# Kernel tuning notes

Measured on AMD Instinct MI355X. Metric: run time of the kernel, lower is better.

The kernel has to match this reference:

```python
import jax, jax.numpy as jnp
import numpy as np

N = 50000      # nodes
E = 400000     # directed edges
F_IN = 128     # input features
H0, C0 = 4, 64     # layer0: 4 heads x 64, concat -> 256
H1, C1 = 1, 256    # layer1: 1 head x 256, mean/concat -> 256
NCLS = 10
SLOPE = 0.2    # PyG GATConv leaky_relu negative_slope


def setup_inputs() -> dict:
    key = jax.random.key(0)
    ks = jax.random.split(key, 20)
    g = lambda k, shape, fan_in: jax.random.normal(k, shape, jnp.float32) * (1.0 / np.sqrt(fan_in))
    x = jax.random.normal(ks[0], (N, F_IN), jnp.float32)
    edge_index = jax.random.randint(ks[1], (2, E), 0, N)
    return {
        "x": x,
        "edge_index": edge_index,
        # GATConv layer 0: 128 -> 4 heads x 64, concat
        "W0": g(ks[2], (F_IN, H0 * C0), F_IN),
        "a_src0": g(ks[3], (H0, C0), C0),
        "a_dst0": g(ks[4], (H0, C0), C0),
        "b0": jnp.zeros((H0 * C0,), jnp.float32),
        # GATConv layer 1: 256 -> 1 head x 256, averaged
        "W1": g(ks[5], (H0 * C0, H1 * C1), H0 * C0),
        "a_src1": g(ks[6], (H1, C1), C1),
        "a_dst1": g(ks[7], (H1, C1), C1),
        "b1": jnp.zeros((C1,), jnp.float32),
        # MLP head 256 -> 512 -> 1024 -> NCLS
        "lw1": g(ks[8], (256, 512), 256), "lb1": jnp.zeros((512,), jnp.float32),
        "lw2": g(ks[9], (512, 1024), 512), "lb2": jnp.zeros((1024,), jnp.float32),
        "lw3": g(ks[10], (1024, NCLS), 1024), "lb3": jnp.zeros((NCLS,), jnp.float32),
    }


def _gat_conv(x, src, dst, valid, W, a_src, a_dst, b, heads, ch, concat):
    """PyG GATConv (eval mode, dropout=0): gather -> edge attention ->
    softmax over incoming edges per target -> scatter-sum aggregate."""
    n = x.shape[0]
    h = (x @ W).reshape(n, heads, ch)                      # [N,H,C]
    alpha_src = jnp.sum(h * a_src[None], axis=-1)          # [N,H]
    alpha_dst = jnp.sum(h * a_dst[None], axis=-1)          # [N,H]
    e = jax.nn.leaky_relu(alpha_src[src] + alpha_dst[dst], SLOPE)  # [Etot,H]
    e = jnp.where(valid[:, None], e, -1e9)                 # removed self-loops
    emax = jax.lax.stop_gradient(jax.ops.segment_max(e, dst, num_segments=n))
    w = jnp.exp(e - emax[dst]) * valid[:, None].astype(e.dtype)
    denom = jax.ops.segment_sum(w, dst, num_segments=n)    # [N,H] (>0: self-loops)
    w = w / denom[dst]
    out = jax.ops.segment_sum(h[src] * w[..., None], dst, num_segments=n)  # [N,H,C]
    out = out.reshape(n, heads * ch) if concat else out.mean(axis=1)
    return out + b


def reference(x, edge_index, W0, a_src0, a_dst0, b0, W1, a_src1, a_dst1, b1,
              lw1, lb1, lw2, lb2, lw3, lb3):
    n = x.shape[0]
    s0, d0 = edge_index[0], edge_index[1]
    loop = jnp.arange(n, dtype=s0.dtype)
    src = jnp.concatenate([s0, loop])
    dst = jnp.concatenate([d0, loop])
    valid = jnp.concatenate([s0 != d0, jnp.ones((n,), bool)])  # remove+add self-loops
    h = jax.nn.relu(_gat_conv(x, src, dst, valid, W0, a_src0, a_dst0, b0, H0, C0, True))
    h = jax.nn.relu(_gat_conv(h, src, dst, valid, W1, a_src1, a_dst1, b1, H1, C1, False))
    h = jax.nn.relu(h @ lw1 + lb1)
    h = jax.nn.relu(h @ lw2 + lb2)
    h = jax.nn.relu(h @ lw3 + lb3)
    return jax.nn.softmax(h, axis=1)
```

## Files before the change

### kernel.cpp

```cpp
#include <hip/hip_runtime.h>
#include <cstdint>
#include <cstddef>

#define F_IN   128
#define SLOPE  0.2f

typedef unsigned short u16;
typedef __attribute__((ext_vector_type(8))) short     bf16x8;
typedef __attribute__((ext_vector_type(8))) unsigned short u16x8;
typedef __attribute__((ext_vector_type(4))) unsigned short u16x4;
typedef __attribute__((ext_vector_type(4))) float     f32x4;

__device__ __forceinline__ u16 f2bf(float f) {
    unsigned u = __float_as_uint(f);
    unsigned r = u + 0x7FFFu + ((u >> 16) & 1u);
    return (u16)(r >> 16);
}
__device__ __forceinline__ float bf2f(u16 h) {
    return __uint_as_float(((unsigned)h) << 16);
}

__device__ __forceinline__ float lrelu(float v) { return v >= 0.f ? v : SLOPE * v; }

__global__ void alphas0_k(const u16* __restrict__ h0, const float* __restrict__ a_src,
                          const float* __restrict__ a_dst, float* __restrict__ asrc,
                          float* __restrict__ adst, int N) {
    int gid = blockIdx.x * blockDim.x + threadIdx.x;
    int n = gid >> 6, lane = gid & 63;
    if (n >= N) return;
    #pragma unroll
    for (int h = 0; h < 4; ++h) {
        float v  = bf2f(h0[(size_t)n * 256 + h * 64 + lane]);
        float s1 = v * a_src[h * 64 + lane];
        float s2 = v * a_dst[h * 64 + lane];
        #pragma unroll
        for (int off = 32; off; off >>= 1) {
            s1 += __shfl_down(s1, off);
            s2 += __shfl_down(s2, off);
        }
        if (lane == 0) { asrc[n * 4 + h] = s1; adst[n * 4 + h] = s2; }
    }
}

__global__ void alphas1_k(const u16* __restrict__ h1, const float* __restrict__ a_src,
                          const float* __restrict__ a_dst, float* __restrict__ asrc,
                          float* __restrict__ adst, int N) {
    int gid = blockIdx.x * blockDim.x + threadIdx.x;
    int n = gid >> 6, lane = gid & 63;
    if (n >= N) return;
    float s1 = 0.f, s2 = 0.f;
    #pragma unroll
    for (int k = 0; k < 4; ++k) {
        float v = bf2f(h1[(size_t)n * 256 + k * 64 + lane]);
        s1 += v * a_src[k * 64 + lane];
        s2 += v * a_dst[k * 64 + lane];
    }
    #pragma unroll
    for (int off = 32; off; off >>= 1) {
        s1 += __shfl_down(s1, off);
        s2 += __shfl_down(s2, off);
    }
    if (lane == 0) { asrc[n] = s1; adst[n] = s2; }
}

__global__ void deg_init(int* __restrict__ deg, int N) {
    int i = blockIdx.x * blockDim.x + threadIdx.x;
    if (i < N) deg[i] = 1;
}

__global__ void count_deg(const int* __restrict__ ei, int* __restrict__ deg, int E) {
    int e = blockIdx.x * blockDim.x + threadIdx.x;
    if (e >= E) return;
    int s = ei[e], d = ei[E + e];
    if (s != d) atomicAdd(&deg[d], 1);
}

__global__ void scan1(const int* __restrict__ deg, int* __restrict__ part,
                      int* __restrict__ bsum, int N) {
    __shared__ int sm[256];
    int i = blockIdx.x * 256 + threadIdx.x;
    int v = (i < N) ? deg[i] : 0;
    sm[threadIdx.x] = v; __syncthreads();
    for (int off = 1; off < 256; off <<= 1) {
        int tv = (threadIdx.x >= off) ? sm[threadIdx.x - off] : 0;
        __syncthreads();
        sm[threadIdx.x] += tv;
        __syncthreads();
    }
    if (i < N) part[i] = sm[threadIdx.x] - v;
    if (threadIdx.x == 255) bsum[blockIdx.x] = sm[255];
}

__global__ void scan2(int* __restrict__ bsum, int nb) {
    __shared__ int sm[256];
    __shared__ int carry;
    if (threadIdx.x == 0) carry = 0;
    __syncthreads();
    for (int base = 0; base < nb; base += 256) {
        int i = base + threadIdx.x;
        int v = (i < nb) ? bsum[i] : 0;
        sm[threadIdx.x] = v; __syncthreads();
        for (int off = 1; off < 256; off <<= 1) {
            int tv = (threadIdx.x >= off) ? sm[threadIdx.x - off] : 0;
            __syncthreads();
            sm[threadIdx.x] += tv;
            __syncthreads();
        }
        if (i < nb) bsum[i] = sm[threadIdx.x] - v + carry;
        __syncthreads();
        if (threadIdx.x == 0) carry += sm[255];
        __syncthreads();
    }
}

__global__ void scan3(const int* __restrict__ deg, const int* __restrict__ part,
                      const int* __restrict__ bsum, int* __restrict__ rowp,
                      int* __restrict__ cursor, int N) {
    int i = blockIdx.x * blockDim.x + threadIdx.x;
    if (i >= N) return;
    int r = part[i] + bsum[i >> 8];
    rowp[i] = r;
    cursor[i] = r;
    if (i == N - 1) rowp[N] = r + deg[i];
}

__global__ void scatter_k(const int* __restrict__ ei, int* __restrict__ cursor,
                          int* __restrict__ csr, int E, int N) {
    int e = blockIdx.x * blockDim.x + threadIdx.x;
    if (e >= E + N) return;
    int s, d;
    if (e < E) { s = ei[e]; d = ei[E + e]; if (s == d) return; }
    else       { s = d = e - E; }
    int pos = atomicAdd(&cursor[d], 1);
    csr[pos] = s;
}

__global__ void gat_gather0(const int* __restrict__ csr, const int* __restrict__ rowp,
                            const u16* __restrict__ h0, const float* __restrict__ asrc,
                            const float* __restrict__ adst, const float* __restrict__ b,
                            float* __restrict__ outx, int N) {
    int gid = blockIdx.x * blockDim.x + threadIdx.x;
    int n = gid >> 6, lane = gid & 63;
    if (n >= N) return;
    int beg = rowp[n], end = rowp[n + 1];
    float4 ad = *(const float4*)(adst + (size_t)n * 4);
    float m0 = -1e30f, m1 = -1e30f, m2 = -1e30f, m3 = -1e30f;
    for (int i = beg + lane; i < end; i += 64) {
        int s = csr[i];
        float4 as = *(const float4*)(asrc + (size_t)s * 4);
        m0 = fmaxf(m0, lrelu(as.x + ad.x));
        m1 = fmaxf(m1, lrelu(as.y + ad.y));
        m2 = fmaxf(m2, lrelu(as.z + ad.z));
        m3 = fmaxf(m3, lrelu(as.w + ad.w));
    }
    #pragma unroll
    for (int off = 32; off; off >>= 1) {
        m0 = fmaxf(m0, __shfl_xor(m0, off));
        m1 = fmaxf(m1, __shfl_xor(m1, off));
        m2 = fmaxf(m2, __shfl_xor(m2, off));
        m3 = fmaxf(m3, __shfl_xor(m3, off));
    }
    float acc0 = 0.f, acc1 = 0.f, acc2 = 0.f, acc3 = 0.f;
    float den0 = 0.f, den1 = 0.f, den2 = 0.f, den3 = 0.f;
    for (int i = beg; i < end; ++i) {
        int s = csr[i];
        float4 as = *(const float4*)(asrc + (size_t)s * 4);
        float w0 = __expf(lrelu(as.x + ad.x) - m0);
        float w1 = __expf(lrelu(as.y + ad.y) - m1);
        float w2 = __expf(lrelu(as.z + ad.z) - m2);
        float w3 = __expf(lrelu(as.w + ad.w) - m3);
        den0 += w0; den1 += w1; den2 += w2; den3 += w3;
        const u16* hs = h0 + (size_t)s * 256;
        acc0 += w0 * bf2f(hs[lane]);
        acc1 += w1 * bf2f(hs[64 + lane]);
        acc2 += w2 * bf2f(hs[128 + lane]);
        acc3 += w3 * bf2f(hs[192 + lane]);
    }
    float* po = outx + (size_t)n * 256;
    float v;
    v = acc0 / den0 + b[lane];       po[lane]       = v > 0.f ? v : 0.f;
    v = acc1 / den1 + b[64 + lane];  po[64 + lane]  = v > 0.f ? v : 0.f;
    v = acc2 / den2 + b[128 + lane]; po[128 + lane] = v > 0.f ? v : 0.f;
    v = acc3 / den3 + b[192 + lane]; po[192 + lane] = v > 0.f ? v : 0.f;
}

__global__ void gat_gather1(const int* __restrict__ csr, const int* __restrict__ rowp,
                            const u16* __restrict__ h1, const float* __restrict__ asrc,
                            const float* __restrict__ adst, const float* __restrict__ b,
                            u16* __restrict__ outx, int N) {
    int gid = blockIdx.x * blockDim.x + threadIdx.x;
    int n = gid >> 6, lane = gid & 63;
    if (n >= N) return;
    int beg = rowp[n], end = rowp[n + 1];
    float adn = adst[n];
    float mx = -1e30f;
    for (int i = beg + lane; i < end; i += 64) {
        int s = csr[i];
        mx = fmaxf(mx, lrelu(asrc[s] + adn));
    }
    #pragma unroll
    for (int off = 32; off; off >>= 1) mx = fmaxf(mx, __shfl_xor(mx, off));
    float acc0 = 0.f, acc1 = 0.f, acc2 = 0.f, acc3 = 0.f, den = 0.f;
    for (int i = beg; i < end; ++i) {
        int s = csr[i];
        float w = __expf(lrelu(asrc[s] + adn) - mx);
        den += w;
        const u16* hs = h1 + (size_t)s * 256;
        acc0 += w * bf2f(hs[lane]);
        acc1 += w * bf2f(hs[64 + lane]);
        acc2 += w * bf2f(hs[128 + lane]);
        acc3 += w * bf2f(hs[192 + lane]);
    }
    float inv = 1.f / den;
    u16* po = outx + (size_t)n * 256;
    float v;
    v = acc0 * inv + b[lane];       po[lane]       = f2bf(v > 0.f ? v : 0.f);
    v = acc1 * inv + b[64 + lane];  po[64 + lane]  = f2bf(v > 0.f ? v : 0.f);
    v = acc2 * inv + b[128 + lane]; po[128 + lane] = f2bf(v > 0.f ? v : 0.f);
    v = acc3 * inv + b[192 + lane]; po[192 + lane] = f2bf(v > 0.f ? v : 0.f);
}

__global__ void pack_w(const float* __restrict__ W, u16* __restrict__ out,
                       int K, int Nsrc, int NT) {
    int gid  = blockIdx.x * blockDim.x + threadIdx.x;
    int lane = gid & 63, frag = gid >> 6;
    int KT = K >> 5;
    if (frag >= KT * NT) return;
    int nt = frag % NT, kt = frag / NT;
    int n  = nt * 16 + (lane & 15);
    int k0 = kt * 32 + ((lane >> 4) << 3);
    u16x8 v8;
    #pragma unroll
    for (int i = 0; i < 8; ++i) {
        float v = (n < Nsrc) ? W[(size_t)(k0 + i) * Nsrc + n] : 0.f;
        v8[i] = f2bf(v);
    }
    *(u16x8*)(out + (size_t)(frag * 64 + lane) * 8) = v8;
}

__global__ void pack_w_hl(const float* __restrict__ W, u16* __restrict__ ohi,
                          u16* __restrict__ olo, int K, int Nsrc, int NT) {
    int gid  = blockIdx.x * blockDim.x + threadIdx.x;
    int lane = gid & 63, frag = gid >> 6;
    int KT = K >> 5;
    if (frag >= KT * NT) return;
    int nt = frag % NT, kt = frag / NT;
    int n  = nt * 16 + (lane & 15);
    int k0 = kt * 32 + ((lane >> 4) << 3);
    u16x8 h8, l8;
    #pragma unroll
    for (int i = 0; i < 8; ++i) {
        float v = (n < Nsrc) ? W[(size_t)(k0 + i) * Nsrc + n] : 0.f;
        u16 hi = f2bf(v);
        h8[i] = hi;
        l8[i] = f2bf(v - bf2f(hi));
    }
    *(u16x8*)(ohi + (size_t)(frag * 64 + lane) * 8) = h8;
    *(u16x8*)(olo + (size_t)(frag * 64 + lane) * 8) = l8;
}

__device__ __forceinline__ bf16x8 lds_afrag(const u16* buf, int Kdim, int row0, int kt, int lane) {
    int row = row0 + (lane & 15);
    int k   = kt * 32 + ((lane >> 4) << 3);
    int idx = (row * Kdim + k) ^ ((row & 7) << 3);
    return *(const bf16x8*)(buf + idx);
}

__global__ __launch_bounds__(512) void gemm_mfma(
    const float* __restrict__ A, const u16* __restrict__ bhi, const u16* __restrict__ blo,
    u16* __restrict__ C, int M, int K) {
    __shared__ __align__(16) u16 Ahi[64 * 256];
    __shared__ __align__(16) u16 Alo[64 * 256];
    int t = threadIdx.x, lane = t & 63, w = t >> 6;
    int row0 = blockIdx.x * 64;
    int K4 = K >> 2;

    for (int idx = t; idx < 64 * K4; idx += 512) {
        int row = idx / K4, kq = (idx % K4) << 2;
        int gr = row0 + row;
        float4 v = make_float4(0.f, 0.f, 0.f, 0.f);
        if (gr < M) v = *(const float4*)(A + (size_t)gr * K + kq);
        u16x4 h4, l4;
        float vv[4] = {v.x, v.y, v.z, v.w};
        #pragma unroll
        for (int i = 0; i < 4; ++i) {
            u16 hi = f2bf(vv[i]);
            h4[i] = hi;
            l4[i] = f2bf(vv[i] - bf2f(hi));
        }
        int sidx = (row * K + kq) ^ ((row & 7) << 3);
        *(u16x4*)(Ahi + sidx) = h4;
        *(u16x4*)(Alo + sidx) = l4;
    }
    __syncthreads();

    int KT = K >> 5;
    f32x4 acc[4][2] = {};
    for (int kt = 0; kt < KT; ++kt) {
        bf16x8 ah[4], al[4];
        #pragma unroll
        for (int mt = 0; mt < 4; ++mt) {
            ah[mt] = lds_afrag(Ahi, K, mt * 16, kt, lane);
            al[mt] = lds_afrag(Alo, K, mt * 16, kt, lane);
        }
        #pragma unroll
        for (int nt = 0; nt < 2; ++nt) {
            int ntg = w * 2 + nt;
            size_t fo = ((size_t)(kt * 16 + ntg) * 64 + lane) * 8;
            bf16x8 bh = *(const bf16x8*)(bhi + fo);
            bf16x8 bl = *(const bf16x8*)(blo + fo);
            #pragma unroll
            for (int mt = 0; mt < 4; ++mt) {
                acc[mt][nt] = __builtin_amdgcn_mfma_f32_16x16x32_bf16(al[mt], bh, acc[mt][nt], 0, 0, 0);
                acc[mt][nt] = __builtin_amdgcn_mfma_f32_16x16x32_bf16(ah[mt], bl, acc[mt][nt], 0, 0, 0);
                acc[mt][nt] = __builtin_amdgcn_mfma_f32_16x16x32_bf16(ah[mt], bh, acc[mt][nt], 0, 0, 0);
            }
        }
    }

    #pragma unroll
    for (int mt = 0; mt < 4; ++mt)
        #pragma unroll
        for (int nt = 0; nt < 2; ++nt) {
            int col = w * 32 + nt * 16 + (lane & 15);
            #pragma unroll
            for (int j = 0; j < 4; ++j) {
                int gr = row0 + mt * 16 + ((lane >> 4) << 2) + j;
                if (gr < M) C[(size_t)gr * 256 + col] = f2bf(acc[mt][nt][j]);
            }
        }
}

#define NB 32

__global__ __launch_bounds__(1024) void mlp_mfma(
    const u16* __restrict__ m0,
    const u16* __restrict__ w1p, const float* __restrict__ lb1,
    const u16* __restrict__ w2p, const float* __restrict__ lb2,
    const u16* __restrict__ w3p, const float* __restrict__ lb3,
    float* __restrict__ out, int N) {
    __shared__ __align__(16) u16 ldsA0[32 * 256];
    __shared__ __align__(16) u16 ldsA1[32 * 512];
    __shared__ __align__(16) u16 ldsA2[32 * 1024];
    __shared__ float slog[32 * 16];

    int t = threadIdx.x, lane = t & 63, w = t >> 6;
    int nb = blockIdx.x * NB;

    if (t < 512) slog[t] = 0.f;

    {
        int row = t >> 5, kb = (t & 31) << 3;
        int gn = nb + row;
        u16x8 v8;
        if (gn < N) v8 = *(const u16x8*)(m0 + (size_t)gn * 256 + kb);
        else        v8 = (u16x8)0;
        int idx = (row * 256 + kb) ^ ((row & 7) << 3);
        *(u16x8*)(ldsA0 + idx) = v8;
    }
    __syncthreads();

    f32x4 acc1[2][2] = {};
    for (int kt = 0; kt < 8; ++kt) {
        bf16x8 a0 = lds_afrag(ldsA0, 256, 0,  kt, lane);
        bf16x8 a1 = lds_afrag(ldsA0, 256, 16, kt, lane);
        #pragma unroll
        for (int nt = 0; nt < 2; ++nt) {
            int ntg = w * 2 + nt;
            bf16x8 b = *(const bf16x8*)(w1p + ((size_t)(kt * 32 + ntg) * 64 + lane) * 8);
            acc1[0][nt] = __builtin_amdgcn_mfma_f32_16x16x32_bf16(a0, b, acc1[0][nt], 0, 0, 0);
            acc1[1][nt] = __builtin_amdgcn_mfma_f32_16x16x32_bf16(a1, b, acc1[1][nt], 0, 0, 0);
        }
    }
    #pragma unroll
    for (int mt = 0; mt < 2; ++mt)
        #pragma unroll
        for (int nt = 0; nt < 2; ++nt) {
            int col = w * 32 + nt * 16 + (lane & 15);
            float bv = lb1[col];
            #pragma unroll
            for (int j = 0; j < 4; ++j) {
                int row = mt * 16 + ((lane >> 4) << 2) + j;
                float v = acc1[mt][nt][j] + bv;
                v = v > 0.f ? v : 0.f;
                ldsA1[(row * 512 + col) ^ ((row & 7) << 3)] = f2bf(v);
            }
        }
    __syncthreads();

    f32x4 acc2[2][4] = {};
    for (int kt = 0; kt < 16; ++kt) {
        bf16x8 a0 = lds_afrag(ldsA1, 512, 0,  kt, lane);
        bf16x8 a1 = lds_afrag(ldsA1, 512, 16, kt, lane);
        #pragma unroll
        for (int nt = 0; nt < 4; ++nt) {
            int ntg = w * 4 + nt;
            bf16x8 b = *(const bf16x8*)(w2p + ((size_t)(kt * 64 + ntg) * 64 + lane) * 8);
            acc2[0][nt] = __builtin_amdgcn_mfma_f32_16x16x32_bf16(a0, b, acc2[0][nt], 0, 0, 0);
            acc2[1][nt] = __builtin_amdgcn_mfma_f32_16x16x32_bf16(a1, b, acc2[1][nt], 0, 0, 0);
        }
    }
    #pragma unroll
    for (int mt = 0; mt < 2; ++mt)
        #pragma unroll
        for (int nt = 0; nt < 4; ++nt) {
            int col = w * 64 + nt * 16 + (lane & 15);
            float bv = lb2[col];
            #pragma unroll
            for (int j = 0; j < 4; ++j) {
                int row = mt * 16 + ((lane >> 4) << 2) + j;
                float v = acc2[mt][nt][j] + bv;
                v = v > 0.f ? v : 0.f;
                ldsA2[(row * 1024 + col) ^ ((row & 7) << 3)] = f2bf(v);
            }
        }
    __syncthreads();

    {
        f32x4 acc[2] = {};
        #pragma unroll
        for (int kk = 0; kk < 2; ++kk) {
            int kt = w * 2 + kk;
            bf16x8 b3 = *(const bf16x8*)(w3p + ((size_t)kt * 64 + lane) * 8);
            bf16x8 a0 = lds_afrag(ldsA2, 1024, 0,  kt, lane);
            bf16x8 a1 = lds_afrag(ldsA2, 1024, 16, kt, lane);
            acc[0] = __builtin_amdgcn_mfma_f32_16x16x32_bf16(a0, b3, acc[0], 0, 0, 0);
            acc[1] = __builtin_amdgcn_mfma_f32_16x16x32_bf16(a1, b3, acc[1], 0, 0, 0);
        }
        int col = lane & 15;
        #pragma unroll
        for (int mt = 0; mt < 2; ++mt)
            #pragma unroll
            for (int j = 0; j < 4; ++j) {
                int row = mt * 16 + ((lane >> 4) << 2) + j;
                atomicAdd(&slog[row * 16 + col], acc[mt][j]);
            }
    }
    __syncthreads();

    if (t < 32) {
        int gn = nb + t;
        if (gn < N) {
            float lg[10], m = -1e30f;
            #pragma unroll
            for (int k = 0; k < 10; ++k) {
                float v = slog[t * 16 + k] + lb3[k];
                v = v > 0.f ? v : 0.f;
                lg[k] = v;
                if (v > m) m = v;
            }
            float ssum = 0.f;
            #pragma unroll
            for (int k = 0; k < 10; ++k) { lg[k] = __expf(lg[k] - m); ssum += lg[k]; }
            float inv = 1.f / ssum;
            #pragma unroll
            for (int k = 0; k < 10; ++k) out[(size_t)gn * 10 + k] = lg[k] * inv;
        }
    }
}

extern "C" void kernel_launch(void* const* d_in, const int* in_sizes, int n_in,
                              void* d_out, int out_size, void* d_ws, size_t ws_size,
                              hipStream_t stream) {
    const float* x       = (const float*)d_in[0];
    const int*   ei      = (const int*)  d_in[1];
    const float* W0      = (const float*)d_in[2];
    const float* a_src0  = (const float*)d_in[3];
    const float* a_dst0  = (const float*)d_in[4];
    const float* b0      = (const float*)d_in[5];
    const float* W1      = (const float*)d_in[6];
    const float* a_src1  = (const float*)d_in[7];
    const float* a_dst1  = (const float*)d_in[8];
    const float* b1      = (const float*)d_in[9];
    const float* lw1     = (const float*)d_in[10];
    const float* lb1     = (const float*)d_in[11];
    const float* lw2     = (const float*)d_in[12];
    const float* lb2     = (const float*)d_in[13];
    const float* lw3     = (const float*)d_in[14];
    const float* lb3     = (const float*)d_in[15];
    float*       out     = (float*)d_out;

    const int N  = in_sizes[0] / F_IN;
    const int E  = in_sizes[1] / 2;
    const int ET = E + N;

    char* base = (char*)d_ws;
    size_t szHb = (size_t)N * 256 * sizeof(u16);
    u16*   hbf  = (u16*)base;
    float* bufG = (float*)(base + szHb);
    u16*   m0b  = (u16*)(base + szHb + (size_t)N * 256 * sizeof(float));
    float* asrc = (float*)(base + 2 * szHb + (size_t)N * 256 * sizeof(float));
    float* adst = asrc + (size_t)N * 4;
    u16*   w1p  = (u16*)(adst + (size_t)N * 4);
    u16*   w2p  = w1p + 256 * 512;
    u16*   w3p  = w2p + 512 * 1024;
    u16*   w0h  = w3p + 1024 * 16;
    u16*   w0l  = w0h + 128 * 256;
    u16*   w1h  = w0l + 128 * 256;
    u16*   w1l  = w1h + 256 * 256;
    int*   deg  = (int*)(w1l + 256 * 256);
    int*   rowp   = deg + N;
    int*   cursor = rowp + N + 1;
    int*   part   = cursor + N;
    int*   bsum   = part + N;
    int*   csr    = bsum + 256;

    const int TB  = 256;
    const int nb1 = (N + 255) / 256;
    const int gemm_grid = (N + 63) / 64;

    pack_w<<<(8  * 32 * 64 + TB - 1) / TB, TB, 0, stream>>>(lw1, w1p, 256,  512,  32);
    pack_w<<<(16 * 64 * 64 + TB - 1) / TB, TB, 0, stream>>>(lw2, w2p, 512,  1024, 64);
    pack_w<<<(32 * 1  * 64 + TB - 1) / TB, TB, 0, stream>>>(lw3, w3p, 1024, 10,   1);
    pack_w_hl<<<(4 * 16 * 64 + TB - 1) / TB, TB, 0, stream>>>(W0, w0h, w0l, 128, 256, 16);
    pack_w_hl<<<(8 * 16 * 64 + TB - 1) / TB, TB, 0, stream>>>(W1, w1h, w1l, 256, 256, 16);

    deg_init<<<nb1, TB, 0, stream>>>(deg, N);
    count_deg<<<(E + TB - 1) / TB, TB, 0, stream>>>(ei, deg, E);
    scan1<<<nb1, TB, 0, stream>>>(deg, part, bsum, N);
    scan2<<<1, TB, 0, stream>>>(bsum, nb1);
    scan3<<<nb1, TB, 0, stream>>>(deg, part, bsum, rowp, cursor, N);
    scatter_k<<<(ET + TB - 1) / TB, TB, 0, stream>>>(ei, cursor, csr, E, N);

    gemm_mfma<<<gemm_grid, 512, 0, stream>>>(x, w0h, w0l, hbf, N, 128);
    alphas0_k<<<(N * 64 + TB - 1) / TB, TB, 0, stream>>>(hbf, a_src0, a_dst0, asrc, adst, N);
    gat_gather0<<<((size_t)N * 64 + TB - 1) / TB, TB, 0, stream>>>(csr, rowp, hbf, asrc, adst, b0, bufG, N);

    gemm_mfma<<<gemm_grid, 512, 0, stream>>>(bufG, w1h, w1l, hbf, N, 256);
    alphas1_k<<<(N * 64 + TB - 1) / TB, TB, 0, stream>>>(hbf, a_src1, a_dst1, asrc, adst, N);
    gat_gather1<<<((size_t)N * 64 + TB - 1) / TB, TB, 0, stream>>>(csr, rowp, hbf, asrc, adst, b1, m0b, N);

    mlp_mfma<<<(N + NB - 1) / NB, 1024, 0, stream>>>(m0b, w1p, lb1, w2p, lb2, w3p, lb3, out, N);
}
```

Measured before the change: 458.3 us.

## Chunk MLP layer2 output and fuse layer3 per chunk, halving block size

```diff
diff --git a/kernel.cpp b/kernel.cpp
--- a/kernel.cpp
+++ b/kernel.cpp
@@ -333,107 +333,115 @@
 
 #define NB 32
 
-__global__ __launch_bounds__(1024) void mlp_mfma(
+__global__ __launch_bounds__(512) void mlp_mfma(
     const u16* __restrict__ m0,
     const u16* __restrict__ w1p, const float* __restrict__ lb1,
     const u16* __restrict__ w2p, const float* __restrict__ lb2,
     const u16* __restrict__ w3p, const float* __restrict__ lb3,
     float* __restrict__ out, int N) {
-    __shared__ __align__(16) u16 ldsA0[32 * 256];
+    __shared__ __align__(16) u16 ldsIn[32 * 256];
     __shared__ __align__(16) u16 ldsA1[32 * 512];
-    __shared__ __align__(16) u16 ldsA2[32 * 1024];
     __shared__ float slog[32 * 16];
 
     int t = threadIdx.x, lane = t & 63, w = t >> 6;
     int nb = blockIdx.x * NB;
 
-    if (t < 512) slog[t] = 0.f;
-
-    {
-        int row = t >> 5, kb = (t & 31) << 3;
+    slog[t] = 0.f;
+
+    #pragma unroll
+    for (int u = 0; u < 2; ++u) {
+        int unit = t + u * 512;
+        int row = unit >> 5, kb = (unit & 31) << 3;
         int gn = nb + row;
         u16x8 v8;
         if (gn < N) v8 = *(const u16x8*)(m0 + (size_t)gn * 256 + kb);
         else        v8 = (u16x8)0;
         int idx = (row * 256 + kb) ^ ((row & 7) << 3);
-        *(u16x8*)(ldsA0 + idx) = v8;
+        *(u16x8*)(ldsIn + idx) = v8;
     }
     __syncthreads();
 
-    f32x4 acc1[2][2] = {};
-    for (int kt = 0; kt < 8; ++kt) {
-        bf16x8 a0 = lds_afrag(ldsA0, 256, 0,  kt, lane);
-        bf16x8 a1 = lds_afrag(ldsA0, 256, 16, kt, lane);
-        #pragma unroll
-        for (int nt = 0; nt < 2; ++nt) {
-            int ntg = w * 2 + nt;
-            bf16x8 b = *(const bf16x8*)(w1p + ((size_t)(kt * 32 + ntg) * 64 + lane) * 8);
-            acc1[0][nt] = __builtin_amdgcn_mfma_f32_16x16x32_bf16(a0, b, acc1[0][nt], 0, 0, 0);
-            acc1[1][nt] = __builtin_amdgcn_mfma_f32_16x16x32_bf16(a1, b, acc1[1][nt], 0, 0, 0);
-        }
-    }
-    #pragma unroll
-    for (int mt = 0; mt < 2; ++mt)
-        #pragma unroll
-        for (int nt = 0; nt < 2; ++nt) {
-            int col = w * 32 + nt * 16 + (lane & 15);
-            float bv = lb1[col];
+    {
+        f32x4 acc1[2][4] = {};
+        for (int kt = 0; kt < 8; ++kt) {
+            bf16x8 a0 = lds_afrag(ldsIn, 256, 0,  kt, lane);
+            bf16x8 a1 = lds_afrag(ldsIn, 256, 16, kt, lane);
+            #pragma unroll
+            for (int nt = 0; nt < 4; ++nt) {
+                int ntg = w * 4 + nt;
+                bf16x8 b = *(const bf16x8*)(w1p + ((size_t)(kt * 32 + ntg) * 64 + lane) * 8);
+                acc1[0][nt] = __builtin_amdgcn_mfma_f32_16x16x32_bf16(a0, b, acc1[0][nt], 0, 0, 0);
+                acc1[1][nt] = __builtin_amdgcn_mfma_f32_16x16x32_bf16(a1, b, acc1[1][nt], 0, 0, 0);
+            }
+        }
+        #pragma unroll
+        for (int mt = 0; mt < 2; ++mt)
+            #pragma unroll
+            for (int nt = 0; nt < 4; ++nt) {
+                int col = w * 64 + nt * 16 + (lane & 15);
+                float bv = lb1[col];
+                #pragma unroll
+                for (int j = 0; j < 4; ++j) {
+                    int row = mt * 16 + ((lane >> 4) << 2) + j;
+                    float v = acc1[mt][nt][j] + bv;
+                    v = v > 0.f ? v : 0.f;
+                    ldsA1[(row * 512 + col) ^ ((row & 7) << 3)] = f2bf(v);
+                }
+            }
+    }
+    __syncthreads();
+
+    bf16x8 b3[4];
+    #pragma unroll
+    for (int ch = 0; ch < 4; ++ch)
+        b3[ch] = *(const bf16x8*)(w3p + ((size_t)(ch * 8 + w) * 64 + lane) * 8);
+
+    f32x4 acc3[2] = {};
+    for (int ch = 0; ch < 4; ++ch) {
+        f32x4 acc[2][2] = {};
+        for (int kt = 0; kt < 16; ++kt) {
+            bf16x8 a0 = lds_afrag(ldsA1, 512, 0,  kt, lane);
+            bf16x8 a1 = lds_afrag(ldsA1, 512, 16, kt, lane);
+            #pragma unroll
+            for (int nt = 0; nt < 2; ++nt) {
+                int ntg = ch * 16 + w * 2 + nt;
+                bf16x8 b = *(const bf16x8*)(w2p + ((size_t)(kt * 64 + ntg) * 64 + lane) * 8);
+                acc[0][nt] = __builtin_amdgcn_mfma_f32_16x16x32_bf16(a0, b, acc[0][nt], 0, 0, 0);
+                acc[1][nt] = __builtin_amdgcn_mfma_f32_16x16x32_bf16(a1, b, acc[1][nt], 0, 0, 0);
+            }
+        }
+        #pragma unroll
+        for (int mt = 0; mt < 2; ++mt)
+            #pragma unroll
+            for (int nt = 0; nt < 2; ++nt) {
+                int lcol = w * 32 + nt * 16 + (lane & 15);
+                float bv = lb2[ch * 256 + lcol];
+                #pragma unroll
+                for (int j = 0; j < 4; ++j) {
+                    int row = mt * 16 + ((lane >> 4) << 2) + j;
+                    float v = acc[mt][nt][j] + bv;
+                    v = v > 0.f ? v : 0.f;
+                    ldsIn[(row * 256 + lcol) ^ ((row & 7) << 3)] = f2bf(v);
+                }
+            }
+        __syncthreads();
+        {
+            bf16x8 a0 = lds_afrag(ldsIn, 256, 0,  w, lane);
+            bf16x8 a1 = lds_afrag(ldsIn, 256, 16, w, lane);
+            acc3[0] = __builtin_amdgcn_mfma_f32_16x16x32_bf16(a0, b3[ch], acc3[0], 0, 0, 0);
+            acc3[1] = __builtin_amdgcn_mfma_f32_16x16x32_bf16(a1, b3[ch], acc3[1], 0, 0, 0);
+        }
+        __syncthreads();
+    }
+
+    {
+        int col = lane & 15;
+        #pragma unroll
+        for (int mt = 0; mt < 2; ++mt)
             #pragma unroll
             for (int j = 0; j < 4; ++j) {
                 int row = mt * 16 + ((lane >> 4) << 2) + j;
-                float v = acc1[mt][nt][j] + bv;
-                v = v > 0.f ? v : 0.f;
-                ldsA1[(row * 512 + col) ^ ((row & 7) << 3)] = f2bf(v);
-            }
-        }
-    __syncthreads();
-
-    f32x4 acc2[2][4] = {};
-    for (int kt = 0; kt < 16; ++kt) {
-        bf16x8 a0 = lds_afrag(ldsA1, 512, 0,  kt, lane);
-        bf16x8 a1 = lds_afrag(ldsA1, 512, 16, kt, lane);
-        #pragma unroll
-        for (int nt = 0; nt < 4; ++nt) {
-            int ntg = w * 4 + nt;
-            bf16x8 b = *(const bf16x8*)(w2p + ((size_t)(kt * 64 + ntg) * 64 + lane) * 8);
-            acc2[0][nt] = __builtin_amdgcn_mfma_f32_16x16x32_bf16(a0, b, acc2[0][nt], 0, 0, 0);
-            acc2[1][nt] = __builtin_amdgcn_mfma_f32_16x16x32_bf16(a1, b, acc2[1][nt], 0, 0, 0);
-        }
-    }
-    #pragma unroll
-    for (int mt = 0; mt < 2; ++mt)
-        #pragma unroll
-        for (int nt = 0; nt < 4; ++nt) {
-            int col = w * 64 + nt * 16 + (lane & 15);
-            float bv = lb2[col];
-            #pragma unroll
-            for (int j = 0; j < 4; ++j) {
-                int row = mt * 16 + ((lane >> 4) << 2) + j;
-                float v = acc2[mt][nt][j] + bv;
-                v = v > 0.f ? v : 0.f;
-                ldsA2[(row * 1024 + col) ^ ((row & 7) << 3)] = f2bf(v);
-            }
-        }
-    __syncthreads();
-
-    {
-        f32x4 acc[2] = {};
-        #pragma unroll
-        for (int kk = 0; kk < 2; ++kk) {
-            int kt = w * 2 + kk;
-            bf16x8 b3 = *(const bf16x8*)(w3p + ((size_t)kt * 64 + lane) * 8);
-            bf16x8 a0 = lds_afrag(ldsA2, 1024, 0,  kt, lane);
-            bf16x8 a1 = lds_afrag(ldsA2, 1024, 16, kt, lane);
-            acc[0] = __builtin_amdgcn_mfma_f32_16x16x32_bf16(a0, b3, acc[0], 0, 0, 0);
-            acc[1] = __builtin_amdgcn_mfma_f32_16x16x32_bf16(a1, b3, acc[1], 0, 0, 0);
-        }
-        int col = lane & 15;
-        #pragma unroll
-        for (int mt = 0; mt < 2; ++mt)
-            #pragma unroll
-            for (int j = 0; j < 4; ++j) {
-                int row = mt * 16 + ((lane >> 4) << 2) + j;
-                atomicAdd(&slog[row * 16 + col], acc[mt][j]);
+                atomicAdd(&slog[row * 16 + col], acc3[mt][j]);
             }
     }
     __syncthreads();
@@ -530,5 +538,5 @@
     alphas1_k<<<(N * 64 + TB - 1) / TB, TB, 0, stream>>>(hbf, a_src1, a_dst1, asrc, adst, N);
     gat_gather1<<<((size_t)N * 64 + TB - 1) / TB, TB, 0, stream>>>(csr, rowp, hbf, asrc, adst, b1, m0b, N);
 
-    mlp_mfma<<<(N + NB - 1) / NB, 1024, 0, stream>>>(m0b, w1p, lb1, w2p, lb2, w3p, lb3, out, N);
-}
+    mlp_mfma<<<(N + NB - 1) / NB, 512, 0, stream>>>(m0b, w1p, lb1, w2p, lb2, w3p, lb3, out, N);
+}
```

New measurement: 532.0 us. 1.16x slower.
